# Optimization experiments

Hardware: AMD Instinct MI355X
Metric: run time of the kernel (lower is better)

## Reference

```python
import jax, jax.numpy as jnp
import numpy as np

B, N, FIN = 32, 1024, 6
KCHEB = 3
CLASS_NUM = 40


def _pairwise_adj(x):
    # x: [B, N, D] -> exp(-squared_euclidean_dist) adjacency [B, N, N]
    inner = jnp.einsum('bnd,bmd->bnm', x, x)
    sq = jnp.sum(x * x, axis=-1)
    d2 = sq[:, :, None] - 2.0 * inner + sq[:, None, :]
    return jnp.exp(-d2)


def _get_laplacian(adj):
    # normalized Laplacian: I - D^{-1/2} A D^{-1/2}
    deg = jnp.sum(adj, axis=-1)                       # [B, N]
    d_is = 1.0 / jnp.sqrt(deg)                        # [B, N]
    eye = jnp.eye(adj.shape[-1], dtype=adj.dtype)
    return eye - d_is[:, :, None] * adj * d_is[:, None, :]


def _cheb_conv(x, L, W, b):
    # Chebyshev graph conv: sum_k T_k(L) x W_k + b;  W: [K, Fin, Fout]
    x0 = x
    x1 = jnp.einsum('bnm,bmf->bnf', L, x0)
    out = jnp.einsum('bnf,fg->bng', x0, W[0]) + jnp.einsum('bnf,fg->bng', x1, W[1])
    xk_2, xk_1 = x0, x1
    for k in range(2, W.shape[0]):
        xk = 2.0 * jnp.einsum('bnm,bmf->bnf', L, xk_1) - xk_2
        out = out + jnp.einsum('bnf,fg->bng', xk, W[k])
        xk_2, xk_1 = xk_1, xk
    return out + b


def setup_inputs() -> dict:
    key = jax.random.key(0)
    ks = jax.random.split(key, 16)

    def w(k, shape, fan_in):
        return jax.random.normal(k, shape, dtype=jnp.float32) / np.sqrt(fan_in)

    return {
        'x': jax.random.normal(ks[0], (B, N, FIN), dtype=jnp.float32),
        'W1': w(ks[1], (KCHEB, 6, 128), 6 * KCHEB),
        'b1': jnp.zeros((128,), jnp.float32),
        'W2': w(ks[2], (KCHEB, 128, 512), 128 * KCHEB),
        'b2': jnp.zeros((512,), jnp.float32),
        'W3': w(ks[3], (KCHEB, 512, 1024), 512 * KCHEB),
        'b3': jnp.zeros((1024,), jnp.float32),
        'fc1_w': w(ks[4], (1024, 512), 1024),
        'fc1_b': jnp.zeros((512,), jnp.float32),
        'fc2_w': w(ks[5], (512, 128), 512),
        'fc2_b': jnp.zeros((128,), jnp.float32),
        'fc3_w': w(ks[6], (128, CLASS_NUM), 128),
        'fc3_b': jnp.zeros((CLASS_NUM,), jnp.float32),
    }


def reference(x, W1, b1, W2, b2, W3, b3, fc1_w, fc1_b, fc2_w, fc2_b, fc3_w, fc3_b):
    # Laplacians are computed under torch.no_grad in the original
    L = _get_laplacian(_pairwise_adj(x))
    out = jax.nn.relu(_cheb_conv(x, L, W1, b1))        # [B, N, 128]

    L = _get_laplacian(_pairwise_adj(out))
    out = jax.nn.relu(_cheb_conv(out, L, W2, b2))      # [B, N, 512]

    L = _get_laplacian(_pairwise_adj(out))
    out = jax.nn.relu(_cheb_conv(out, L, W3, b3))      # [B, N, 1024]

    out = jnp.max(out, axis=1)                          # global max pool -> [B, 1024]
    out = jax.nn.relu(out @ fc1_w + fc1_b)              # dropout is identity at eval
    out = jax.nn.relu(out @ fc2_w + fc2_b)
    out = out @ fc3_w + fc3_b                           # [B, CLASS_NUM]
    return out
```

## Files before the change

kernel.cpp:

```cpp
#include <hip/hip_runtime.h>
#include <cstddef>


#define NN 1024

typedef unsigned short ushort_t;
typedef __bf16 bf16x8 __attribute__((ext_vector_type(8)));
typedef float f32x4 __attribute__((ext_vector_type(4)));

__device__ inline ushort_t f2bf(float f) {
    unsigned int u = __float_as_uint(f);
    u = (u + 0x7fffu + ((u >> 16) & 1u)) >> 16;
    return (ushort_t)u;
}
__device__ inline float bf2f(ushort_t s) {
    return __uint_as_float(((unsigned int)s) << 16);
}

__device__ __attribute__((always_inline)) inline void gld16(
    const ushort_t* g, ushort_t* l) {
    __builtin_amdgcn_global_load_lds(
        (__attribute__((address_space(1))) void*)(ushort_t*)g,
        (__attribute__((address_space(3))) void*)l, 16, 0, 0);
}

__global__ void zero_kernel(float* __restrict__ p, int n) {
    int i = blockIdx.x * blockDim.x + threadIdx.x;
    if (i < n) p[i] = 0.f;
}

__global__ __launch_bounds__(256) void wconvT_kernel(
    const float* __restrict__ W, ushort_t* __restrict__ Wt, int Fi, int Fo, int Ks) {
    int p = blockIdx.z;
    int k0 = blockIdx.y * 64, g0 = blockIdx.x * 64;
    __shared__ float T[64][65];
    int t = threadIdx.x;
#pragma unroll
    for (int q = 0; q < 16; ++q) {
        int kr = (t >> 6) + 4 * q, gc = t & 63;
        int k = k0 + kr, g = g0 + gc;
        T[kr][gc] = (k < Fi && g < Fo) ? W[((size_t)p * Fi + k) * Fo + g] : 0.f;
    }
    __syncthreads();
#pragma unroll
    for (int q = 0; q < 16; ++q) {
        int gr = (t >> 6) + 4 * q, kc = t & 63;
        int g = g0 + gr, k = k0 + kc;
        if (g < Fo && k < Ks)
            Wt[((size_t)p * Fo + g) * Ks + k] = f2bf(T[kc][gr]);
    }
}

__global__ __launch_bounds__(256) void prep2_kernel(
    const float* __restrict__ X, ushort_t* __restrict__ hi, ushort_t* __restrict__ lo,
    ushort_t* __restrict__ Xt, float* __restrict__ sq, int F, int Fp, int bsh) {
    int L = blockIdx.x;
    int b = L & ((1 << bsh) - 1), n0 = (L >> bsh) * 64;
    int t = threadIdx.x;
    __shared__ float T[64][65];
    __shared__ float red[4][64];
    const float* Xb = X + ((size_t)b * NN + n0) * F;
    float sacc = 0.f;

    for (int f0 = 0; f0 < Fp; f0 += 64) {
        __syncthreads();
#pragma unroll
        for (int p = 0; p < 16; ++p) {
            int nr = (t >> 6) + 4 * p, fc = t & 63;
            int f = f0 + fc;
            T[nr][fc] = (f < F) ? Xb[(size_t)nr * F + f] : 0.f;
        }
        __syncthreads();
#pragma unroll
        for (int p = 0; p < 16; ++p) {
            int nr = (t >> 6) + 4 * p, fc = t & 63;
            int f = f0 + fc;
            if (f < Fp) {
                float x = T[nr][fc];
                ushort_t h = f2bf(x);
                size_t off = ((size_t)b * NN + n0 + nr) * Fp + f;
                hi[off] = h;
                lo[off] = f2bf(x - bf2f(h));
            }
        }
#pragma unroll
        for (int p = 0; p < 16; ++p) {
            int fr = (t >> 6) + 4 * p;
            int f = f0 + fr;
            if (f < F)
                Xt[((size_t)b * Fp + f) * NN + n0 + (t & 63)] = f2bf(T[t & 63][fr]);
        }
        {
            int nl = t & 63, fq = t >> 6;
#pragma unroll
            for (int fc = 0; fc < 16; ++fc) {
                float v = T[nl][fq * 16 + fc];
                sacc += v * v;
            }
        }
    }
    red[t >> 6][t & 63] = sacc;
    __syncthreads();
    if (t < 64)
        sq[(size_t)b * NN + n0 + t] = red[0][t] + red[1][t] + red[2][t] + red[3][t];
}

__global__ __launch_bounds__(256) void adj_kernel(
    const ushort_t* __restrict__ hi, const ushort_t* __restrict__ lo,
    const float* __restrict__ sq, ushort_t* __restrict__ Abf,
    float* __restrict__ deg_part, int Fp, int bsh, int BCv) {
    int t = threadIdx.x;
    int L = blockIdx.x;
    int b = L & ((1 << bsh) - 1);
    int rest = L >> bsh;
    int m0 = (rest & 7) * 128, n0 = (rest >> 3) * 128;
    const ushort_t* Hb = hi + (size_t)b * NN * Fp;
    const ushort_t* Lb = lo + (size_t)b * NN * Fp;
    ushort_t* Ab = Abf + (size_t)b * NN * NN;
    const float* sqb = sq + (size_t)b * NN;

    int lane = t & 63, quad = lane >> 4, l16 = lane & 15, wave = t >> 6;
    int rowoff = (wave >> 1) * 64, coloff = (wave & 1) * 64;

    __shared__ __align__(16) ushort_t smem[40960];

    f32x4 acc[4][4];
#pragma unroll
    for (int i = 0; i < 4; ++i)
#pragma unroll
        for (int j = 0; j < 4; ++j) acc[i][j] = (f32x4){0.f, 0.f, 0.f, 0.f};

    int rr0 = t >> 2, kq = (t & 3) * 8;
    int rr1 = rr0 + 64;
    const ushort_t* pAh0 = Hb + (size_t)(n0 + rr0) * Fp + kq;
    const ushort_t* pAh1 = Hb + (size_t)(n0 + rr1) * Fp + kq;
    const ushort_t* pAl0 = Lb + (size_t)(n0 + rr0) * Fp + kq;
    const ushort_t* pAl1 = Lb + (size_t)(n0 + rr1) * Fp + kq;
    const ushort_t* pBh0 = Hb + (size_t)(m0 + rr0) * Fp + kq;
    const ushort_t* pBh1 = Hb + (size_t)(m0 + rr1) * Fp + kq;
    const ushort_t* pBl0 = Lb + (size_t)(m0 + rr0) * Fp + kq;
    const ushort_t* pBl1 = Lb + (size_t)(m0 + rr1) * Fp + kq;
    int o0 = rr0 * 40 + kq, o1 = rr1 * 40 + kq;

    {
        *(uint4*)&smem[o0]         = *(const uint4*)pAh0;
        *(uint4*)&smem[o1]         = *(const uint4*)pAh1;
        *(uint4*)&smem[5120 + o0]  = *(const uint4*)pAl0;
        *(uint4*)&smem[5120 + o1]  = *(const uint4*)pAl1;
        *(uint4*)&smem[10240 + o0] = *(const uint4*)pBh0;
        *(uint4*)&smem[10240 + o1] = *(const uint4*)pBh1;
        *(uint4*)&smem[15360 + o0] = *(const uint4*)pBl0;
        *(uint4*)&smem[15360 + o1] = *(const uint4*)pBl1;
    }
    __syncthreads();

    int NIT = Fp >> 5;
    for (int it = 0; it < NIT; ++it) {
        int cur = (it & 1) * 20480;
        int nxt = 20480 - cur;
        uint4 rh0, rh1, rl0, rl1, sh0, sh1, sl0, sl1;
        if (it + 1 < NIT) {
            int k = (it + 1) * 32;
            rh0 = *(const uint4*)(pAh0 + k); rh1 = *(const uint4*)(pAh1 + k);
            rl0 = *(const uint4*)(pAl0 + k); rl1 = *(const uint4*)(pAl1 + k);
            sh0 = *(const uint4*)(pBh0 + k); sh1 = *(const uint4*)(pBh1 + k);
            sl0 = *(const uint4*)(pBl0 + k); sl1 = *(const uint4*)(pBl1 + k);
        }
        ushort_t* Ah = smem + cur;
        ushort_t* Al = smem + cur + 5120;
        ushort_t* Bh = smem + cur + 10240;
        ushort_t* Bl = smem + cur + 15360;
        bf16x8 ah[4], al[4], bh[4], bl[4];
#pragma unroll
        for (int i = 0; i < 4; ++i) {
            ah[i] = *(const bf16x8*)&Ah[(rowoff + i * 16 + l16) * 40 + quad * 8];
            al[i] = *(const bf16x8*)&Al[(rowoff + i * 16 + l16) * 40 + quad * 8];
        }
#pragma unroll
        for (int j = 0; j < 4; ++j) {
            bh[j] = *(const bf16x8*)&Bh[(coloff + j * 16 + l16) * 40 + quad * 8];
            bl[j] = *(const bf16x8*)&Bl[(coloff + j * 16 + l16) * 40 + quad * 8];
        }
#pragma unroll
        for (int i = 0; i < 4; ++i)
#pragma unroll
            for (int j = 0; j < 4; ++j) {
                acc[i][j] = __builtin_amdgcn_mfma_f32_16x16x32_bf16(al[i], bh[j], acc[i][j], 0, 0, 0);
                acc[i][j] = __builtin_amdgcn_mfma_f32_16x16x32_bf16(ah[i], bl[j], acc[i][j], 0, 0, 0);
                acc[i][j] = __builtin_amdgcn_mfma_f32_16x16x32_bf16(ah[i], bh[j], acc[i][j], 0, 0, 0);
            }
        if (it + 1 < NIT) {
            *(uint4*)&smem[nxt + o0]         = rh0;
            *(uint4*)&smem[nxt + o1]         = rh1;
            *(uint4*)&smem[nxt + 5120 + o0]  = rl0;
            *(uint4*)&smem[nxt + 5120 + o1]  = rl1;
            *(uint4*)&smem[nxt + 10240 + o0] = sh0;
            *(uint4*)&smem[nxt + 10240 + o1] = sh1;
            *(uint4*)&smem[nxt + 15360 + o0] = sl0;
            *(uint4*)&smem[nxt + 15360 + o1] = sl1;
        }
        __syncthreads();
    }

    float rs[4][4];
#pragma unroll
    for (int i = 0; i < 4; ++i)
#pragma unroll
        for (int r = 0; r < 4; ++r) rs[i][r] = 0.f;

#pragma unroll
    for (int j = 0; j < 4; ++j) {
        int m = m0 + coloff + j * 16 + l16;
        float sm = sqb[m];
#pragma unroll
        for (int i = 0; i < 4; ++i) {
#pragma unroll
            for (int r = 0; r < 4; ++r) {
                int n = n0 + rowoff + i * 16 + quad * 4 + r;
                float v = __expf(2.f * acc[i][j][r] - sqb[n] - sm);
                Ab[(size_t)n * NN + m] = f2bf(v);
                rs[i][r] += v;
            }
        }
    }
    int slot = (rest & 7) * 2 + (wave & 1);
#pragma unroll
    for (int i = 0; i < 4; ++i)
#pragma unroll
        for (int r = 0; r < 4; ++r) {
            float s = rs[i][r];
            s += __shfl_xor(s, 1);
            s += __shfl_xor(s, 2);
            s += __shfl_xor(s, 4);
            s += __shfl_xor(s, 8);
            if (l16 == 0)
                deg_part[((size_t)slot * BCv + b) * NN + n0 + rowoff + i * 16 + quad * 4 + r] = s;
        }
}

__global__ __launch_bounds__(256) void disscale_kernel(
    ushort_t* __restrict__ Xt, const float* __restrict__ deg_part,
    float* __restrict__ dis, int Fp, int bsh, int BCv) {
    int L = blockIdx.x;
    int b = L & ((1 << bsh) - 1), n0 = (L >> bsh) * 64;
    int t = threadIdx.x;
    __shared__ float dloc[64];
    if (t < 64) {
        float s = 0.f;
#pragma unroll
        for (int k = 0; k < 16; ++k) s += deg_part[((size_t)k * BCv + b) * NN + n0 + t];
        float d = rsqrtf(s);
        dloc[t] = d;
        dis[(size_t)b * NN + n0 + t] = d;
    }
    __syncthreads();
    int lane = t & 63, fq = t >> 6;
    float d = dloc[lane];
    ushort_t* Xb = Xt + (size_t)b * Fp * NN + n0 + lane;
    for (int f = fq; f < Fp; f += 4) {
        size_t off = (size_t)f * NN;
        Xb[off] = f2bf(bf2f(Xb[off]) * d);
    }
}

__global__ __launch_bounds__(256) void lx_kernel(
    const ushort_t* __restrict__ Abf, const float* __restrict__ dis,
    const ushort_t* __restrict__ in_t, const ushort_t* __restrict__ x0t,
    ushort_t* __restrict__ out_t, ushort_t* __restrict__ out_b,
    int F, int Fp, int mode, int ft, int bsh) {
    int t = threadIdx.x;
    int L = blockIdx.x;
    int b = L & ((1 << bsh) - 1);
    int rest = L >> bsh;
    int m0 = (rest % ft) * 128;
    int n0 = (rest / ft) * 64;
    const ushort_t* Ain = in_t + (size_t)b * Fp * NN;
    const ushort_t* Ab = Abf + (size_t)b * NN * NN;

    int lane = t & 63, quad = lane >> 4, l16 = lane & 15, wave = t >> 6;
    int rowoff = wave * 32;

    __shared__ __align__(16) ushort_t smem[18432];

    f32x4 acc[2][4];
#pragma unroll
    for (int i = 0; i < 2; ++i)
#pragma unroll
        for (int j = 0; j < 4; ++j) acc[i][j] = (f32x4){0.f, 0.f, 0.f, 0.f};

    int lr = lane >> 2, lk = (lane & 3) * 8;
    int rbase = wave * 32;
    const ushort_t* gA = Ain + (size_t)(m0 + rbase + lr) * NN + lk;
    const ushort_t* gB = Ab + (size_t)(n0 + wave * 16 + lr) * NN + lk;

#define LX_STAGE(BOFF, CI)                                            \
    {                                                                 \
        int k_ = (CI) * 32;                                           \
        ushort_t* As_ = smem + (BOFF);                                \
        gld16(gA + k_, As_ + rbase * 32);                             \
        gld16(gA + (size_t)16 * NN + k_, As_ + rbase * 32 + 512);     \
        gld16(gB + k_, As_ + 4096 + wave * 16 * 32);                  \
    }
#define LX_COMP(BOFF)                                                            \
    {                                                                            \
        ushort_t* As_ = smem + (BOFF);                                           \
        ushort_t* Bs_ = As_ + 4096;                                              \
        bf16x8 af[2], bfv[4];                                                    \
        _Pragma("unroll")                                                        \
        for (int i = 0; i < 2; ++i)                                              \
            af[i] = *(const bf16x8*)&As_[(rowoff + i * 16 + l16) * 32 + quad * 8]; \
        _Pragma("unroll")                                                        \
        for (int j = 0; j < 4; ++j)                                              \
            bfv[j] = *(const bf16x8*)&Bs_[(j * 16 + l16) * 32 + quad * 8];       \
        _Pragma("unroll")                                                        \
        for (int i = 0; i < 2; ++i)                                              \
            _Pragma("unroll")                                                    \
            for (int j = 0; j < 4; ++j)                                          \
                acc[i][j] = __builtin_amdgcn_mfma_f32_16x16x32_bf16(af[i], bfv[j], acc[i][j], 0, 0, 0); \
    }

    LX_STAGE(0, 0);
    LX_STAGE(6144, 1);
    int cur = 0;
    for (int ci = 0; ci < 32; ++ci) {
        if (ci < 31) { asm volatile("s_waitcnt vmcnt(3)" ::: "memory"); }
        else         { asm volatile("s_waitcnt vmcnt(0)" ::: "memory"); }
        __builtin_amdgcn_s_barrier();
        asm volatile("" ::: "memory");
        if (ci + 2 < 32) {
            int noff = cur + 12288; if (noff >= 18432) noff -= 18432;
            LX_STAGE(noff, ci + 2);
        }
        LX_COMP(cur);
        cur += 6144; if (cur >= 18432) cur = 0;
    }
#undef LX_STAGE
#undef LX_COMP
    __syncthreads();

#pragma unroll
    for (int j = 0; j < 4; ++j) {
        int nl = j * 16 + l16;
        int n = n0 + nl;
        float dn = dis[(size_t)b * NN + n];
        float inv = 1.f / dn;
        float dn2 = dn * dn;
#pragma unroll
        for (int i = 0; i < 2; ++i) {
#pragma unroll
            for (int r = 0; r < 4; ++r) {
                int fl = rowoff + i * 16 + quad * 4 + r;
                int f = m0 + fl;
                float o = 0.f;
                if (f < F) {
                    float a = acc[i][j][r];
                    size_t off = (size_t)f * NN + n;
                    float xin = bf2f(Ain[off]);
                    if (mode == 0) {
                        out_t[(size_t)b * Fp * NN + off] = f2bf(xin - dn2 * a);
                        o = inv * xin - dn * a;
                    } else {
                        float x0 = bf2f(x0t[(size_t)b * Fp * NN + off]);
                        o = inv * (2.f * xin - x0) - 2.f * dn * a;
                    }
                }
                smem[nl * 128 + (((fl >> 3) ^ (nl & 7)) << 3) + (fl & 7)] = f2bf(o);
            }
        }
    }
    __syncthreads();
    for (int s2 = t; s2 < 1024; s2 += 256) {
        int nl = s2 >> 4, oct = s2 & 15;
        int fg = m0 + oct * 8;
        if (fg < Fp) {
            uint4 v = *(const uint4*)&smem[nl * 128 + ((oct ^ (nl & 7)) << 3)];
            *(uint4*)(out_b + ((size_t)b * NN + n0 + nl) * Fp + fg) = v;
        }
    }
}

__global__ __launch_bounds__(512) void proj_kernel(
    const ushort_t* __restrict__ X0, const ushort_t* __restrict__ X1,
    const ushort_t* __restrict__ X2, const ushort_t* __restrict__ Wt,
    const float* __restrict__ bias, float* __restrict__ O, float* __restrict__ pool,
    int Fp, int Fo, int b0, int n_g, int bsh) {
    int t = threadIdx.x;
    int L = blockIdx.x;
    int c = L & ((1 << bsh) - 1);
    int rest = L >> bsh;
    int g0 = (rest % n_g) * 128;
    int r0 = (c * 4 + rest / n_g) * 256;
    int lane = t & 63, quad = lane >> 4, l16 = lane & 15, wave = t >> 6;
    int rowoff = (wave >> 1) * 64, coloff = (wave & 1) * 64;

    __shared__ __align__(16) ushort_t smem[36864];

    f32x4 acc[4][4];
#pragma unroll
    for (int i = 0; i < 4; ++i)
#pragma unroll
        for (int j = 0; j < 4; ++j) acc[i][j] = (f32x4){0.f, 0.f, 0.f, 0.f};

    int lr = lane >> 2, lk = (lane & 3) * 8;
    int nk = Fp >> 5;
    int NIT = 3 * nk;
    size_t FoFp = (size_t)Fo * Fp;
    size_t r16 = (size_t)16 * Fp;

#define PJ_STAGE(BOFF, CI)                                                    \
    {                                                                         \
        int p_ = (CI) / nk;                                                   \
        int k_ = ((CI) - p_ * nk) * 32 + lk;                                  \
        const ushort_t* Xp_ = (p_ == 0) ? X0 : ((p_ == 1) ? X1 : X2);         \
        const ushort_t* ga_ = Xp_ + (size_t)(r0 + wave * 32 + lr) * Fp + k_;  \
        const ushort_t* gb_ = Wt + (size_t)p_ * FoFp +                        \
                              (size_t)(g0 + wave * 16 + lr) * Fp + k_;        \
        ushort_t* As_ = smem + (BOFF) + wave * 1024;                          \
        ushort_t* Bs_ = smem + (BOFF) + 8192 + wave * 512;                    \
        gld16(ga_, As_);                                                      \
        gld16(ga_ + r16, As_ + 512);                                          \
        gld16(gb_, Bs_);                                                      \
    }
#define PJ_COMP(BOFF)                                                           \
    {                                                                           \
        ushort_t* As_ = smem + (BOFF);                                          \
        ushort_t* Bs_ = As_ + 8192;                                             \
        bf16x8 af[4], bfv[4];                                                   \
        _Pragma("unroll")                                                       \
        for (int i = 0; i < 4; ++i)                                             \
            af[i] = *(const bf16x8*)&As_[(rowoff + i * 16 + l16) * 32 + quad * 8];  \
        _Pragma("unroll")                                                       \
        for (int j = 0; j < 4; ++j)                                             \
            bfv[j] = *(const bf16x8*)&Bs_[(coloff + j * 16 + l16) * 32 + quad * 8]; \
        _Pragma("unroll")                                                       \
        for (int i = 0; i < 4; ++i)                                             \
            _Pragma("unroll")                                                   \
            for (int j = 0; j < 4; ++j)                                         \
                acc[i][j] = __builtin_amdgcn_mfma_f32_16x16x32_bf16(af[i], bfv[j], acc[i][j], 0, 0, 0); \
    }

    PJ_STAGE(0, 0);
    PJ_STAGE(12288, 1);
    int cur = 0;
    for (int ci = 0; ci < NIT; ++ci) {
        if (ci < NIT - 1) { asm volatile("s_waitcnt vmcnt(3)" ::: "memory"); }
        else              { asm volatile("s_waitcnt vmcnt(0)" ::: "memory"); }
        __builtin_amdgcn_s_barrier();
        asm volatile("" ::: "memory");
        if (ci + 2 < NIT) {
            int noff = cur + 24576; if (noff >= 36864) noff -= 36864;
            PJ_STAGE(noff, ci + 2);
        }
        PJ_COMP(cur);
        cur += 12288; if (cur >= 36864) cur = 0;
    }
#undef PJ_STAGE
#undef PJ_COMP

    float bias_l[4];
#pragma unroll
    for (int j = 0; j < 4; ++j) bias_l[j] = bias[g0 + coloff + j * 16 + l16];

    if (O) {
#pragma unroll
        for (int i = 0; i < 4; ++i) {
#pragma unroll
            for (int r = 0; r < 4; ++r) {
                int row = r0 + rowoff + i * 16 + quad * 4 + r;
#pragma unroll
                for (int j = 0; j < 4; ++j) {
                    int g = g0 + coloff + j * 16 + l16;
                    O[(size_t)row * Fo + g] = fmaxf(acc[i][j][r] + bias_l[j], 0.f);
                }
            }
        }
    } else {
        float mj[4];
#pragma unroll
        for (int j = 0; j < 4; ++j) {
            float m = 0.f;
#pragma unroll
            for (int i = 0; i < 4; ++i)
#pragma unroll
                for (int r = 0; r < 4; ++r)
                    m = fmaxf(m, acc[i][j][r] + bias_l[j]);
            m = fmaxf(m, 0.f);
            m = fmaxf(m, __shfl_xor(m, 16));
            m = fmaxf(m, __shfl_xor(m, 32));
            mj[j] = m;
        }
        if (quad == 0) {
            int smp = b0 + (r0 >> 10);
#pragma unroll
            for (int j = 0; j < 4; ++j)
                atomicMax((int*)&pool[(size_t)smp * 1024 + g0 + coloff + j * 16 + l16],
                          __float_as_int(mj[j]));
        }
    }
}

__global__ __launch_bounds__(256) void fc_kernel(
    const float* __restrict__ In, const float* __restrict__ W,
    const float* __restrict__ bias, float* __restrict__ out,
    int K, int Nout, int relu) {
    int r = blockIdx.y;
    int c0 = blockIdx.x * 64;
    int t = threadIdx.x;
    int cl = t & 63, ks = t >> 6;
    int c = c0 + cl;
    int kchunk = K >> 2;
    int k0 = ks * kchunk, k1 = k0 + kchunk;
    float s = 0.f;
    if (c < Nout) {
        const float* ip = In + (size_t)r * K;
        const float* wp = W + c;
#pragma unroll 4
        for (int k = k0; k < k1; ++k) s += ip[k] * wp[(size_t)k * Nout];
    }
    __shared__ float red[4][64];
    red[ks][cl] = s;
    __syncthreads();
    if (t < 64 && c0 + t < Nout) {
        float v = red[0][t] + red[1][t] + red[2][t] + red[3][t] + bias[c0 + t];
        if (relu) v = fmaxf(v, 0.f);
        out[(size_t)r * Nout + c0 + t] = v;
    }
}

extern "C" void kernel_launch(void* const* d_in, const int* in_sizes, int n_in,
                              void* d_out, int out_size, void* d_ws, size_t ws_size,
                              hipStream_t stream) {
    const float* x    = (const float*)d_in[0];
    const float* W1   = (const float*)d_in[1];
    const float* b1   = (const float*)d_in[2];
    const float* W2   = (const float*)d_in[3];
    const float* b2   = (const float*)d_in[4];
    const float* W3   = (const float*)d_in[5];
    const float* b3   = (const float*)d_in[6];
    const float* fc1w = (const float*)d_in[7];
    const float* fc1b = (const float*)d_in[8];
    const float* fc2w = (const float*)d_in[9];
    const float* fc2b = (const float*)d_in[10];
    const float* fc3w = (const float*)d_in[11];
    const float* fc3b = (const float*)d_in[12];
    float* out = (float*)d_out;

    auto need = [](size_t BCv) -> size_t {
        size_t us = (size_t)BCv * 1024;
        return 2 * (us * 1024) + 10 * (us * 512) + 2 * 1781760ull +
               4 * (us * 128) + 4 * (us * 512) + 4 * us + 64 * us + 4 * us +
               4 * (32768ull + 16384 + 4096) + 256;
    };
    int BCv = (ws_size >= need(16)) ? 16 : 8;
    int NCH = 32 / BCv;
    int bsh = (BCv == 16) ? 4 : 3;

    size_t usc = (size_t)BCv * 1024;
    size_t Asz = usc * 1024;
    size_t SLv = usc * 512;
    ushort_t* Abf  = (ushort_t*)d_ws;
    ushort_t* X0hi = Abf + Asz;
    ushort_t* X0lo = X0hi + SLv;
    ushort_t* X0t  = X0lo + SLv;
    ushort_t* X1t  = X0t + SLv;
    ushort_t* X1b  = X1t + SLv;
    ushort_t* Wt   = X1b + SLv;
    float* O1   = (float*)(Wt + 1781760);
    float* O2   = O1 + usc * 128;
    float* sq   = O2 + usc * 512;
    float* degp = sq + usc;
    float* dis  = degp + 16 * usc;
    float* pool = dis + usc;
    float* f1   = pool + 32768;
    float* f2   = f1 + 16384;
    ushort_t* X2b = X0lo;

    wconvT_kernel<<<dim3(2, 1, 3), 256, 0, stream>>>(W1, Wt, 6, 128, 32);
    wconvT_kernel<<<dim3(8, 2, 3), 256, 0, stream>>>(W2, Wt + 12288, 128, 512, 128);
    wconvT_kernel<<<dim3(16, 8, 3), 256, 0, stream>>>(W3, Wt + 208896, 512, 1024, 512);
    zero_kernel<<<128, 256, 0, stream>>>(pool, 32768);

    for (int c = 0; c < NCH; ++c) {
        int b0 = c * BCv;
        struct LayerDef {
            const float* X; int F, Fp, Fo;
            const ushort_t* Wtl; const float* bias; float* O;
        };
        LayerDef L[3] = {
            { x + (size_t)b0 * NN * 6, 6,   32,  128,  Wt,          b1, O1 },
            { O1,                      128, 128, 512,  Wt + 12288,  b2, O2 },
            { O2,                      512, 512, 1024, Wt + 208896, b3, nullptr },
        };
        for (int li = 0; li < 3; ++li) {
            LayerDef& Ld = L[li];
            int F = Ld.F, Fp = Ld.Fp;
            int ft = (F + 127) / 128;
            int n_g = Ld.Fo / 128;
            prep2_kernel<<<16 * BCv, 256, 0, stream>>>(Ld.X, X0hi, X0lo, X0t, sq, F, Fp, bsh);
            adj_kernel<<<64 * BCv, 256, 0, stream>>>(X0hi, X0lo, sq, Abf, degp, Fp, bsh, BCv);
            disscale_kernel<<<16 * BCv, 256, 0, stream>>>(X0t, degp, dis, Fp, bsh, BCv);
            lx_kernel<<<ft * 16 * BCv, 256, 0, stream>>>(
                Abf, dis, X0t, nullptr, X1t, X1b, F, Fp, 0, ft, bsh);
            lx_kernel<<<ft * 16 * BCv, 256, 0, stream>>>(
                Abf, dis, X1t, X0t, nullptr, X2b, F, Fp, 1, ft, bsh);
            proj_kernel<<<n_g * 4 * BCv, 512, 0, stream>>>(
                X0hi, X1b, X2b, Ld.Wtl, Ld.bias, Ld.O, pool, Fp, Ld.Fo, b0, n_g, bsh);
        }
    }

    fc_kernel<<<dim3(8, 32), 256, 0, stream>>>(pool, fc1w, fc1b, f1, 1024, 512, 1);
    fc_kernel<<<dim3(2, 32), 256, 0, stream>>>(f1, fc2w, fc2b, f2, 512, 128, 1);
    fc_kernel<<<dim3(1, 32), 256, 0, stream>>>(f2, fc3w, fc3b, out, 128, 40, 0);
}
```

Before: 968.9 us.

## Exploit adjacency symmetry: compute only upper-triangular tiles and mirror them

The adjacency kernel now launches 36 tile blocks per batch instead of 64, covering only the upper-triangular 128x128 tiles of the 8x8 tile grid. Each off-diagonal block also stages its bf16 exp values transposed in shared memory, writes the mirrored tile with coalesced 16-byte stores, and emits column-sum degree partials for the mirrored rows. This removes nearly half of the split-precision MFMA Gram work and exp evaluations. In exchange it adds a shared-memory transpose, an extra barrier and a serial loop to map the block index to a tile, and the diagonal blocks do less work than the others, so the load is uneven.

```diff
diff --git a/kernel.cpp b/kernel.cpp
--- a/kernel.cpp
+++ b/kernel.cpp
@@ -113,7 +113,10 @@
     int L = blockIdx.x;
     int b = L & ((1 << bsh) - 1);
     int rest = L >> bsh;
-    int m0 = (rest & 7) * 128, n0 = (rest >> 3) * 128;
+    int ti = 0;
+    while (rest >= 8 - ti) { rest -= 8 - ti; ++ti; }
+    int tj = ti + rest;
+    int n0 = ti * 128, m0 = tj * 128;
     const ushort_t* Hb = hi + (size_t)b * NN * Fp;
     const ushort_t* Lb = lo + (size_t)b * NN * Fp;
     ushort_t* Ab = Abf + (size_t)b * NN * NN;
@@ -202,7 +205,9 @@
         __syncthreads();
     }
 
+    bool offdiag = (ti != tj);
     float rs[4][4];
+    float cs[4] = {0.f, 0.f, 0.f, 0.f};
 #pragma unroll
     for (int i = 0; i < 4; ++i)
 #pragma unroll
@@ -210,20 +215,26 @@
 
 #pragma unroll
     for (int j = 0; j < 4; ++j) {
-        int m = m0 + coloff + j * 16 + l16;
+        int ml = coloff + j * 16 + l16;
+        int m = m0 + ml;
         float sm = sqb[m];
 #pragma unroll
         for (int i = 0; i < 4; ++i) {
 #pragma unroll
             for (int r = 0; r < 4; ++r) {
-                int n = n0 + rowoff + i * 16 + quad * 4 + r;
+                int nl = rowoff + i * 16 + quad * 4 + r;
+                int n = n0 + nl;
                 float v = __expf(2.f * acc[i][j][r] - sqb[n] - sm);
                 Ab[(size_t)n * NN + m] = f2bf(v);
                 rs[i][r] += v;
+                if (offdiag) {
+                    cs[j] += v;
+                    smem[ml * 128 + (((nl >> 3) ^ (ml & 7)) << 3) + (nl & 7)] = f2bf(v);
+                }
             }
         }
     }
-    int slot = (rest & 7) * 2 + (wave & 1);
+    int slot = tj * 2 + (wave & 1);
 #pragma unroll
     for (int i = 0; i < 4; ++i)
 #pragma unroll
@@ -236,6 +247,28 @@
             if (l16 == 0)
                 deg_part[((size_t)slot * BCv + b) * NN + n0 + rowoff + i * 16 + quad * 4 + r] = s;
         }
+
+    if (offdiag) {
+#pragma unroll
+        for (int j = 0; j < 4; ++j) {
+            float s = cs[j];
+            s += __shfl_xor(s, 16);
+            s += __shfl_xor(s, 32);
+            cs[j] = s;
+        }
+        if (quad == 0) {
+#pragma unroll
+            for (int j = 0; j < 4; ++j)
+                deg_part[((size_t)(ti * 2 + (wave >> 1)) * BCv + b) * NN +
+                         m0 + coloff + j * 16 + l16] = cs[j];
+        }
+        __syncthreads();
+        for (int s2 = t; s2 < 2048; s2 += 256) {
+            int ml = s2 >> 4, oct = s2 & 15;
+            uint4 v4 = *(const uint4*)&smem[ml * 128 + ((oct ^ (ml & 7)) << 3)];
+            *(uint4*)(Ab + (size_t)(m0 + ml) * NN + n0 + oct * 8) = v4;
+        }
+    }
 }
 
 __global__ __launch_bounds__(256) void disscale_kernel(
@@ -597,7 +630,7 @@
             int ft = (F + 127) / 128;
             int n_g = Ld.Fo / 128;
             prep2_kernel<<<16 * BCv, 256, 0, stream>>>(Ld.X, X0hi, X0lo, X0t, sq, F, Fp, bsh);
-            adj_kernel<<<64 * BCv, 256, 0, stream>>>(X0hi, X0lo, sq, Abf, degp, Fp, bsh, BCv);
+            adj_kernel<<<36 * BCv, 256, 0, stream>>>(X0hi, X0lo, sq, Abf, degp, Fp, bsh, BCv);
             disscale_kernel<<<16 * BCv, 256, 0, stream>>>(X0t, degp, dis, Fp, bsh, BCv);
             lx_kernel<<<ft * 16 * BCv, 256, 0, stream>>>(
                 Abf, dis, X0t, nullptr, X1t, X1b, F, Fp, 0, ft, bsh);
```

After: 957.1 us. No clear change (-1.2%).
